# Performance work log

Hardware: AMD Instinct MI355X
Metric: run time of the kernel (lower is better)

Reference implementation:

```python
import jax, jax.numpy as jnp
import numpy as np

N = 50000      # nodes
E = 400000     # edges (avg degree 8)
N_IN = 256     # n_in_chan
N_HID = 256    # n_hid_chan


def gcn_conv(x, src, dst, W, b, n):
    """PyG GCNConv: D^{-1/2}(A+I)D^{-1/2} X W^T + b (add_self_loops=True, unit weights)."""
    h = x @ W.T                                           # [n, out]
    # degree over A + I: each node has a self loop (the initial ones) plus in-edges
    deg = jnp.ones((n,), h.dtype).at[dst].add(1.0)        # [n]
    dinv = jax.lax.rsqrt(deg)                             # deg >= 1 always
    norm = dinv[src] * dinv[dst]                          # [E]
    agg = jnp.zeros_like(h).at[dst].add(h[src] * norm[:, None])
    agg = agg + h * (dinv * dinv)[:, None]                # self-loop term, norm = dinv_i^2
    return agg + b


def setup_inputs() -> dict:
    key = jax.random.key(0)
    k1, k2, k3, k4 = jax.random.split(key, 4)
    x = jax.random.normal(k1, (N, N_IN + N_HID), dtype=jnp.float32)
    edge_index = jax.random.randint(k2, (2, E), 0, N, dtype=jnp.int64)
    s1 = 1.0 / np.sqrt(N_IN + N_HID)
    s2 = 1.0 / np.sqrt(N_HID)
    W1 = jax.random.normal(k3, (N_HID, N_IN + N_HID), dtype=jnp.float32) * s1
    W2 = jax.random.normal(k4, (N_HID, N_HID), dtype=jnp.float32) * s2
    b1 = jnp.zeros((N_HID,), jnp.float32)
    b2 = jnp.zeros((N_HID,), jnp.float32)
    return {"x": x, "edge_index": edge_index, "W1": W1, "b1": b1, "W2": W2, "b2": b2}


def reference(x, edge_index, W1, b1, W2, b2):
    src, dst = edge_index[0], edge_index[1]
    h = jax.nn.relu(gcn_conv(x, src, dst, W1, b1, N))
    return gcn_conv(h, src, dst, W2, b2, N)
```

## Files before the change

kernel.cpp:

```cpp
#include <hip/hip_runtime.h>
#include <hip/hip_bf16.h>

#define NN 50000
#define CH 256
#define SLOTS 96

typedef unsigned short u16;
typedef unsigned int   u32;

using short8 = __attribute__((ext_vector_type(8))) short;
using u16x8  = __attribute__((ext_vector_type(8))) unsigned short;
using f32x4  = __attribute__((ext_vector_type(4))) float;

static __device__ __forceinline__ float4 ld4(const float* p){ return *(const float4*)p; }

static __device__ __forceinline__ u16 f2b(float f){
  u32 u = __float_as_uint(f);
  u = (u + 0x7fffu + ((u >> 16) & 1u)) >> 16;
  return (u16)u;
}
static __device__ __forceinline__ float b2f(u16 b){
  return __uint_as_float(((u32)b) << 16);
}
static __device__ __forceinline__ int pkbf(float lo, float hi){
  __hip_bfloat162 h = __float22bfloat162_rn(make_float2(lo, hi));
  int r; __builtin_memcpy(&r, &h, 4); return r;
}


__global__ void ell_build_kernel(const int* __restrict__ src, const int* __restrict__ dst,
                                 int* __restrict__ deg, int* __restrict__ ell, int E,
                                 const float* __restrict__ W2, u16* __restrict__ W2bf, int w2n4){
  int T = gridDim.x * 256;
  int g = blockIdx.x*256 + threadIdx.x;
  if (g < E){
    int d = dst[g];
    int pos = atomicAdd(&deg[d], 1);
    if (pos < SLOTS) ell[(size_t)d*SLOTS + pos] = src[g];
  }
  for (int i = g; i < w2n4; i += T){
    float4 v = ld4(W2 + (size_t)i*4);
    ushort4 o; o.x=f2b(v.x); o.y=f2b(v.y); o.z=f2b(v.z); o.w=f2b(v.w);
    *(ushort4*)(W2bf + (size_t)i*4) = o;
  }
}


__global__ __launch_bounds__(256) void gemm_f32in_db_kernel(const float* __restrict__ A,
                                                            const float* __restrict__ B,
                                                            u16* __restrict__ C,
                                                            int M, int K){
  __shared__ u16 As[2][128*32];
  __shared__ u16 Bs[2][128*32];
  int tid = threadIdx.x;
  int wave = tid >> 6, lane = tid & 63;
  int bm = blockIdx.x, bn = blockIdx.y;

  int sr = tid >> 2;
  int sc = (tid & 3) * 8;
  int rA0 = bm*128 + sr;       if (rA0 > M-1) rA0 = M-1;
  int rA1 = bm*128 + 64 + sr;  if (rA1 > M-1) rA1 = M-1;
  const float* ga0 = A + (size_t)rA0*K + sc;
  const float* ga1 = A + (size_t)rA1*K + sc;
  const float* gb0 = B + (size_t)(bn*128 + sr)*K + sc;
  const float* gb1 = B + (size_t)(bn*128 + 64 + sr)*K + sc;

  int wm = wave & 1, wn = wave >> 1;
  int lm = lane & 15;
  int lk = (lane >> 4) * 8;

  f32x4 acc[4][4] = {};

  float4 a00,a01,a10,a11,b00,b01,b10,b11;
  auto LOADR = [&](int k0){
    a00 = ld4(ga0 + k0); a01 = ld4(ga0 + k0 + 4);
    a10 = ld4(ga1 + k0); a11 = ld4(ga1 + k0 + 4);
    b00 = ld4(gb0 + k0); b01 = ld4(gb0 + k0 + 4);
    b10 = ld4(gb1 + k0); b11 = ld4(gb1 + k0 + 4);
  };
  auto STORE = [&](int buf){
    int4 wa0 = { pkbf(a00.x,a00.y), pkbf(a00.z,a00.w), pkbf(a01.x,a01.y), pkbf(a01.z,a01.w) };
    int4 wa1 = { pkbf(a10.x,a10.y), pkbf(a10.z,a10.w), pkbf(a11.x,a11.y), pkbf(a11.z,a11.w) };
    int4 wb0 = { pkbf(b00.x,b00.y), pkbf(b00.z,b00.w), pkbf(b01.x,b01.y), pkbf(b01.z,b01.w) };
    int4 wb1 = { pkbf(b10.x,b10.y), pkbf(b10.z,b10.w), pkbf(b11.x,b11.y), pkbf(b11.z,b11.w) };
    *(int4*)&As[buf][(size_t)sr*32 + sc]      = wa0;
    *(int4*)&As[buf][(size_t)(64+sr)*32 + sc] = wa1;
    *(int4*)&Bs[buf][(size_t)sr*32 + sc]      = wb0;
    *(int4*)&Bs[buf][(size_t)(64+sr)*32 + sc] = wb1;
  };

  const int NIT = K >> 5;
  LOADR(0);
  STORE(0);
  if (NIT > 1) LOADR(32);
  __syncthreads();

  for (int it = 0; it < NIT; ++it){
    int buf = it & 1;
    short8 af[4], bfr[4];
    #pragma unroll
    for (int i=0;i<4;i++)
      af[i] = *(const short8*)&As[buf][(size_t)(wm*64 + i*16 + lm)*32 + lk];
    #pragma unroll
    for (int j=0;j<4;j++)
      bfr[j] = *(const short8*)&Bs[buf][(size_t)(wn*64 + j*16 + lm)*32 + lk];
    #pragma unroll
    for (int i=0;i<4;i++)
      #pragma unroll
      for (int j=0;j<4;j++)
        acc[i][j] = __builtin_amdgcn_mfma_f32_16x16x32_bf16(af[i], bfr[j], acc[i][j], 0, 0, 0);
    if (it + 1 < NIT){
      STORE(buf ^ 1);
      if (it + 2 < NIT) LOADR((it+2)*32);
    }
    __syncthreads();
  }

  int rb = (lane >> 4) * 4;
  #pragma unroll
  for (int i=0;i<4;i++){
    #pragma unroll
    for (int r=0;r<4;r++){
      int row = bm*128 + wm*64 + i*16 + rb + r;
      if (row < M){
        #pragma unroll
        for (int j=0;j<4;j++){
          int col = bn*128 + wn*64 + j*16 + lm;
          C[(size_t)row*CH + col] = f2b(acc[i][j][r]);
        }
      }
    }
  }
}


static __device__ __forceinline__ void gload_lds16(const u16* g, u16* l){
  __builtin_amdgcn_global_load_lds((const __attribute__((address_space(1))) void*)g,
                                   (__attribute__((address_space(3))) void*)l, 16, 0, 0);
}

__global__ __launch_bounds__(256) void gemm_mfma_kernel(const u16* __restrict__ A,
                                                        const u16* __restrict__ B,
                                                        u16* __restrict__ C,
                                                        int M, int K){
  __shared__ u16 As[128*32];
  __shared__ u16 Bs[128*32];
  int tid = threadIdx.x;
  int wave = tid >> 6, lane = tid & 63;
  int bm = blockIdx.x, bn = blockIdx.y;

  int sr = tid >> 2;
  int sc = (tid & 3) * 8;
  int ar0 = bm*128 + sr;       if (ar0 > M-1) ar0 = M-1;
  int ar1 = bm*128 + 64 + sr;  if (ar1 > M-1) ar1 = M-1;
  const u16* ga0 = A + (size_t)ar0*K + sc;
  const u16* ga1 = A + (size_t)ar1*K + sc;
  const u16* gb0 = B + (size_t)(bn*128 + sr)*K + sc;
  const u16* gb1 = B + (size_t)(bn*128 + 64 + sr)*K + sc;
  u16* la0 = As + (size_t)(wave*64)*8;
  u16* la1 = As + (size_t)(256 + wave*64)*8;
  u16* lb0 = Bs + (size_t)(wave*64)*8;
  u16* lb1 = Bs + (size_t)(256 + wave*64)*8;

  int wm = wave & 1, wn = wave >> 1;
  int lm = lane & 15;
  int lk = (lane >> 4) * 8;

  f32x4 acc[4][4] = {};

  for (int k0 = 0; k0 < K; k0 += 32){
    gload_lds16(ga0 + k0, la0);
    gload_lds16(ga1 + k0, la1);
    gload_lds16(gb0 + k0, lb0);
    gload_lds16(gb1 + k0, lb1);
    __syncthreads();
    short8 af[4], bfr[4];
    #pragma unroll
    for (int i=0;i<4;i++)
      af[i] = *(const short8*)&As[(size_t)(wm*64 + i*16 + lm)*32 + lk];
    #pragma unroll
    for (int j=0;j<4;j++)
      bfr[j] = *(const short8*)&Bs[(size_t)(wn*64 + j*16 + lm)*32 + lk];
    #pragma unroll
    for (int i=0;i<4;i++)
      #pragma unroll
      for (int j=0;j<4;j++)
        acc[i][j] = __builtin_amdgcn_mfma_f32_16x16x32_bf16(af[i], bfr[j], acc[i][j], 0, 0, 0);
    __syncthreads();
  }

  int rb = (lane >> 4) * 4;
  #pragma unroll
  for (int i=0;i<4;i++){
    #pragma unroll
    for (int r=0;r<4;r++){
      int row = bm*128 + wm*64 + i*16 + rb + r;
      if (row < M){
        #pragma unroll
        for (int j=0;j<4;j++){
          int col = bn*128 + wn*64 + j*16 + lm;
          C[(size_t)row*CH + col] = f2b(acc[i][j][r]);
        }
      }
    }
  }
}


template<bool RELU, bool OUTBF>
__global__ __launch_bounds__(256) void aggregate_kernel(const u16* __restrict__ h,
                                                        const float* __restrict__ bias,
                                                        const int* __restrict__ deg,
                                                        const int* __restrict__ ell,
                                                        void* __restrict__ outv, int n){
  int wave = threadIdx.x >> 6;
  int lane = threadIdx.x & 63;
  int i = blockIdx.x*4 + wave;
  if (i >= n) return;
  int half = lane >> 5;
  int c = (lane & 31) * 8;

  int degi = deg[i];
  float di = rsqrtf(1.0f + (float)degi);
  int m = degi < SLOTS ? degi : SLOTS;
  const int* row = ell + (size_t)i*SLOTS;

  float acc[8];
  #pragma unroll
  for (int k=0;k<8;k++) acc[k] = 0.f;

  int e = half;
  for (; e + 6 < m; e += 8){
    int s0 = row[e],   s1 = row[e+2], s2 = row[e+4], s3 = row[e+6];
    float n0 = rsqrtf(1.0f + (float)deg[s0]) * di;
    float n1 = rsqrtf(1.0f + (float)deg[s1]) * di;
    float n2 = rsqrtf(1.0f + (float)deg[s2]) * di;
    float n3 = rsqrtf(1.0f + (float)deg[s3]) * di;
    u16x8 h0 = *(const u16x8*)(h + (size_t)s0*CH + c);
    u16x8 h1 = *(const u16x8*)(h + (size_t)s1*CH + c);
    u16x8 h2 = *(const u16x8*)(h + (size_t)s2*CH + c);
    u16x8 h3 = *(const u16x8*)(h + (size_t)s3*CH + c);
    #pragma unroll
    for (int k=0;k<8;k++) acc[k] += b2f(h0[k])*n0;
    #pragma unroll
    for (int k=0;k<8;k++) acc[k] += b2f(h1[k])*n1;
    #pragma unroll
    for (int k=0;k<8;k++) acc[k] += b2f(h2[k])*n2;
    #pragma unroll
    for (int k=0;k<8;k++) acc[k] += b2f(h3[k])*n3;
  }
  for (; e < m; e += 2){
    int s0 = row[e];
    float n0 = rsqrtf(1.0f + (float)deg[s0]) * di;
    u16x8 h0 = *(const u16x8*)(h + (size_t)s0*CH + c);
    #pragma unroll
    for (int k=0;k<8;k++) acc[k] += b2f(h0[k])*n0;
  }

  if (half == 0){
    float w = di*di;
    float4 b0 = ld4(bias + c), b1 = ld4(bias + c + 4);
    u16x8 hv = *(const u16x8*)(h + (size_t)i*CH + c);
    acc[0] += b2f(hv[0])*w + b0.x; acc[1] += b2f(hv[1])*w + b0.y;
    acc[2] += b2f(hv[2])*w + b0.z; acc[3] += b2f(hv[3])*w + b0.w;
    acc[4] += b2f(hv[4])*w + b1.x; acc[5] += b2f(hv[5])*w + b1.y;
    acc[6] += b2f(hv[6])*w + b1.z; acc[7] += b2f(hv[7])*w + b1.w;
  }

  #pragma unroll
  for (int k=0;k<8;k++) acc[k] += __shfl_xor(acc[k], 32, 64);

  if (half == 0){
    if (RELU){
      #pragma unroll
      for (int k=0;k<8;k++) acc[k] = fmaxf(acc[k], 0.f);
    }
    if (OUTBF){
      u16x8 o;
      #pragma unroll
      for (int k=0;k<8;k++) o[k] = f2b(acc[k]);
      *(u16x8*)((u16*)outv + (size_t)i*CH + c) = o;
    } else {
      float* op = (float*)outv + (size_t)i*CH + c;
      *(float4*)op       = make_float4(acc[0],acc[1],acc[2],acc[3]);
      *(float4*)(op + 4) = make_float4(acc[4],acc[5],acc[6],acc[7]);
    }
  }
}


extern "C" void kernel_launch(void* const* d_in, const int* in_sizes, int n_in,
                              void* d_out, int out_size, void* d_ws, size_t ws_size,
                              hipStream_t stream){
  const float* x  = (const float*)d_in[0];
  const int*   ei = (const int*)d_in[1];
  const float* W1 = (const float*)d_in[2];
  const float* b1 = (const float*)d_in[3];
  const float* W2 = (const float*)d_in[4];
  const float* b2 = (const float*)d_in[5];
  float* out = (float*)d_out;

  const int n = NN;
  const int E = in_sizes[1] / 2;
  const int* src = ei;
  const int* dst = ei + E;
  const int KIN = in_sizes[0] / n;

  char* ws = (char*)d_ws;
  size_t off = 0;
  auto alloc = [&](size_t bytes)->char* {
    char* p = ws + off;
    off += (bytes + 255) & ~(size_t)255;
    return p;
  };
  u16*   h1bf   = (u16*)  alloc((size_t)n*CH*sizeof(u16));
  u16*   g2out  = (u16*)  alloc((size_t)n*CH*sizeof(u16));
  u16*   W2bf   = (u16*)  alloc((size_t)CH*CH*sizeof(u16));
  int*   deg    = (int*)  alloc((size_t)n*sizeof(int));
  int*   ell    = (int*)  alloc((size_t)n*SLOTS*sizeof(int));
  (void)ws_size;

  u16* g1out = (u16*)d_out;

  hipMemsetAsync(deg, 0, (size_t)n*sizeof(int), stream);
  ell_build_kernel<<<(E+255)/256, 256, 0, stream>>>(src, dst, deg, ell, E, W2, W2bf, CH*CH/4);

  dim3 gg((n+127)/128, CH/128);
  gemm_f32in_db_kernel<<<gg, 256, 0, stream>>>(x, W1, g1out, n, KIN);
  aggregate_kernel<true, true><<<(n+3)/4, 256, 0, stream>>>(g1out, b1, deg, ell, h1bf, n);

  gemm_mfma_kernel<<<gg, 256, 0, stream>>>(h1bf, W2bf, g2out, n, CH);
  aggregate_kernel<false, false><<<(n+3)/4, 256, 0, stream>>>(g2out, b2, deg, ell, out, n);
}
```

Before: 316.7 us.

## Shrink GEMM1 M-tile with deeper register prefetch; double-buffer GEMM2 LDS loads

GEMM1 drops its M tile from 128 to 64 rows per block and sets a launch-bounds occupancy hint of 4. It keeps two register stages of fp32 prefetch ahead of the bf16 LDS store, so global loads have more latency cover and more blocks fit per CU. GEMM2 now double-buffers its direct global-to-LDS loads, so the next K tile is fetched while MFMAs run on the current one. The cost is more LDS in GEMM2, lower reuse of B in GEMM1, and a GEMM1 loop unrolled by two that assumes an even tile count.

Result: slower. 328.8 us (+3.8%).

```diff
diff --git a/kernel.cpp b/kernel.cpp
--- a/kernel.cpp
+++ b/kernel.cpp
@@ -46,82 +46,91 @@
 }
 
 
-__global__ __launch_bounds__(256) void gemm_f32in_db_kernel(const float* __restrict__ A,
-                                                            const float* __restrict__ B,
-                                                            u16* __restrict__ C,
-                                                            int M, int K){
-  __shared__ u16 As[2][128*32];
+#define G1_LOAD(S, k0) do{                                              \
+    A##S##a = ld4(ga + (k0));      A##S##b = ld4(ga + (k0) + 4);        \
+    B##S##a = ld4(gb + (k0));      B##S##b = ld4(gb + (k0) + 4);        \
+    B##S##c = ld4(gb + (k0) + 8);  B##S##d = ld4(gb + (k0) + 12);       \
+  }while(0)
+
+#define G1_STORE(S, buf) do{                                            \
+    int4 wa = { pkbf(A##S##a.x,A##S##a.y), pkbf(A##S##a.z,A##S##a.w),   \
+                pkbf(A##S##b.x,A##S##b.y), pkbf(A##S##b.z,A##S##b.w) }; \
+    *(int4*)&As[buf][aoff] = wa;                                        \
+    int4 wb0 = { pkbf(B##S##a.x,B##S##a.y), pkbf(B##S##a.z,B##S##a.w),  \
+                 pkbf(B##S##b.x,B##S##b.y), pkbf(B##S##b.z,B##S##b.w) };\
+    int4 wb1 = { pkbf(B##S##c.x,B##S##c.y), pkbf(B##S##c.z,B##S##c.w),  \
+                 pkbf(B##S##d.x,B##S##d.y), pkbf(B##S##d.z,B##S##d.w) };\
+    *(int4*)&Bs[buf][boff]     = wb0;                                   \
+    *(int4*)&Bs[buf][boff + 8] = wb1;                                   \
+  }while(0)
+
+#define G1_COMPUTE(buf) do{                                             \
+    short8 af[2], bfr[4];                                               \
+    _Pragma("unroll")                                                   \
+    for (int i=0;i<2;i++)                                               \
+      af[i] = *(const short8*)&As[buf][(wm*32 + i*16 + lm)*32 + lk];    \
+    _Pragma("unroll")                                                   \
+    for (int j=0;j<4;j++)                                               \
+      bfr[j] = *(const short8*)&Bs[buf][(wn*64 + j*16 + lm)*32 + lk];   \
+    _Pragma("unroll")                                                   \
+    for (int i=0;i<2;i++)                                               \
+      _Pragma("unroll")                                                 \
+      for (int j=0;j<4;j++)                                             \
+        acc[i][j] = __builtin_amdgcn_mfma_f32_16x16x32_bf16(af[i], bfr[j], acc[i][j], 0, 0, 0); \
+  }while(0)
+
+__global__ __launch_bounds__(256, 4) void gemm1_kernel(const float* __restrict__ A,
+                                                       const float* __restrict__ B,
+                                                       u16* __restrict__ C,
+                                                       int M, int K){
+  __shared__ u16 As[2][64*32];
   __shared__ u16 Bs[2][128*32];
   int tid = threadIdx.x;
   int wave = tid >> 6, lane = tid & 63;
   int bm = blockIdx.x, bn = blockIdx.y;
 
-  int sr = tid >> 2;
-  int sc = (tid & 3) * 8;
-  int rA0 = bm*128 + sr;       if (rA0 > M-1) rA0 = M-1;
-  int rA1 = bm*128 + 64 + sr;  if (rA1 > M-1) rA1 = M-1;
-  const float* ga0 = A + (size_t)rA0*K + sc;
-  const float* ga1 = A + (size_t)rA1*K + sc;
-  const float* gb0 = B + (size_t)(bn*128 + sr)*K + sc;
-  const float* gb1 = B + (size_t)(bn*128 + 64 + sr)*K + sc;
+  int arow = bm*64 + (tid >> 2); if (arow > M-1) arow = M-1;
+  int akc  = (tid & 3) * 8;
+  const float* ga = A + (size_t)arow*K + akc;
+  int brow = bn*128 + (tid >> 1);
+  int bkc  = (tid & 1) * 16;
+  const float* gb = B + (size_t)brow*K + bkc;
+  int aoff = (tid>>2)*32 + akc;
+  int boff = (tid>>1)*32 + bkc;
 
   int wm = wave & 1, wn = wave >> 1;
   int lm = lane & 15;
   int lk = (lane >> 4) * 8;
 
-  f32x4 acc[4][4] = {};
-
-  float4 a00,a01,a10,a11,b00,b01,b10,b11;
-  auto LOADR = [&](int k0){
-    a00 = ld4(ga0 + k0); a01 = ld4(ga0 + k0 + 4);
-    a10 = ld4(ga1 + k0); a11 = ld4(ga1 + k0 + 4);
-    b00 = ld4(gb0 + k0); b01 = ld4(gb0 + k0 + 4);
-    b10 = ld4(gb1 + k0); b11 = ld4(gb1 + k0 + 4);
-  };
-  auto STORE = [&](int buf){
-    int4 wa0 = { pkbf(a00.x,a00.y), pkbf(a00.z,a00.w), pkbf(a01.x,a01.y), pkbf(a01.z,a01.w) };
-    int4 wa1 = { pkbf(a10.x,a10.y), pkbf(a10.z,a10.w), pkbf(a11.x,a11.y), pkbf(a11.z,a11.w) };
-    int4 wb0 = { pkbf(b00.x,b00.y), pkbf(b00.z,b00.w), pkbf(b01.x,b01.y), pkbf(b01.z,b01.w) };
-    int4 wb1 = { pkbf(b10.x,b10.y), pkbf(b10.z,b10.w), pkbf(b11.x,b11.y), pkbf(b11.z,b11.w) };
-    *(int4*)&As[buf][(size_t)sr*32 + sc]      = wa0;
-    *(int4*)&As[buf][(size_t)(64+sr)*32 + sc] = wa1;
-    *(int4*)&Bs[buf][(size_t)sr*32 + sc]      = wb0;
-    *(int4*)&Bs[buf][(size_t)(64+sr)*32 + sc] = wb1;
-  };
+  f32x4 acc[2][4] = {};
+
+  float4 A0a,A0b,B0a,B0b,B0c,B0d;
+  float4 A1a,A1b,B1a,B1b,B1c,B1d;
 
   const int NIT = K >> 5;
-  LOADR(0);
-  STORE(0);
-  if (NIT > 1) LOADR(32);
+  G1_LOAD(0, 0);
+  G1_LOAD(1, 32);
+  G1_STORE(0, 0);
+  G1_LOAD(0, 64);
   __syncthreads();
 
-  for (int it = 0; it < NIT; ++it){
-    int buf = it & 1;
-    short8 af[4], bfr[4];
-    #pragma unroll
-    for (int i=0;i<4;i++)
-      af[i] = *(const short8*)&As[buf][(size_t)(wm*64 + i*16 + lm)*32 + lk];
-    #pragma unroll
-    for (int j=0;j<4;j++)
-      bfr[j] = *(const short8*)&Bs[buf][(size_t)(wn*64 + j*16 + lm)*32 + lk];
-    #pragma unroll
-    for (int i=0;i<4;i++)
-      #pragma unroll
-      for (int j=0;j<4;j++)
-        acc[i][j] = __builtin_amdgcn_mfma_f32_16x16x32_bf16(af[i], bfr[j], acc[i][j], 0, 0, 0);
-    if (it + 1 < NIT){
-      STORE(buf ^ 1);
-      if (it + 2 < NIT) LOADR((it+2)*32);
-    }
+  for (int it = 0; it < NIT; it += 2){
+    G1_COMPUTE(0);
+    G1_STORE(1, 1);
+    if (it + 3 < NIT) G1_LOAD(1, (it+3)*32);
+    __syncthreads();
+    G1_COMPUTE(1);
+    if (it + 2 < NIT) G1_STORE(0, 0);
+    if (it + 4 < NIT) G1_LOAD(0, (it+4)*32);
     __syncthreads();
   }
 
   int rb = (lane >> 4) * 4;
   #pragma unroll
-  for (int i=0;i<4;i++){
+  for (int i=0;i<2;i++){
     #pragma unroll
     for (int r=0;r<4;r++){
-      int row = bm*128 + wm*64 + i*16 + rb + r;
+      int row = bm*64 + wm*32 + i*16 + rb + r;
       if (row < M){
         #pragma unroll
         for (int j=0;j<4;j++){
@@ -143,8 +152,8 @@
                                                         const u16* __restrict__ B,
                                                         u16* __restrict__ C,
                                                         int M, int K){
-  __shared__ u16 As[128*32];
-  __shared__ u16 Bs[128*32];
+  __shared__ u16 As[2][128*32];
+  __shared__ u16 Bs[2][128*32];
   int tid = threadIdx.x;
   int wave = tid >> 6, lane = tid & 63;
   int bm = blockIdx.x, bn = blockIdx.y;
@@ -157,10 +166,8 @@
   const u16* ga1 = A + (size_t)ar1*K + sc;
   const u16* gb0 = B + (size_t)(bn*128 + sr)*K + sc;
   const u16* gb1 = B + (size_t)(bn*128 + 64 + sr)*K + sc;
-  u16* la0 = As + (size_t)(wave*64)*8;
-  u16* la1 = As + (size_t)(256 + wave*64)*8;
-  u16* lb0 = Bs + (size_t)(wave*64)*8;
-  u16* lb1 = Bs + (size_t)(256 + wave*64)*8;
+  int la0 = wave*512;
+  int la1 = 2048 + wave*512;
 
   int wm = wave & 1, wn = wave >> 1;
   int lm = lane & 15;
@@ -168,19 +175,29 @@
 
   f32x4 acc[4][4] = {};
 
-  for (int k0 = 0; k0 < K; k0 += 32){
-    gload_lds16(ga0 + k0, la0);
-    gload_lds16(ga1 + k0, la1);
-    gload_lds16(gb0 + k0, lb0);
-    gload_lds16(gb1 + k0, lb1);
-    __syncthreads();
+  const int NT = K >> 5;
+  gload_lds16(ga0, &As[0][la0]);
+  gload_lds16(ga1, &As[0][la1]);
+  gload_lds16(gb0, &Bs[0][la0]);
+  gload_lds16(gb1, &Bs[0][la1]);
+  __syncthreads();
+
+  for (int t = 0; t < NT; ++t){
+    int buf = t & 1;
+    if (t + 1 < NT){
+      int k0 = (t+1)*32;
+      gload_lds16(ga0 + k0, &As[buf^1][la0]);
+      gload_lds16(ga1 + k0, &As[buf^1][la1]);
+      gload_lds16(gb0 + k0, &Bs[buf^1][la0]);
+      gload_lds16(gb1 + k0, &Bs[buf^1][la1]);
+    }
     short8 af[4], bfr[4];
     #pragma unroll
     for (int i=0;i<4;i++)
-      af[i] = *(const short8*)&As[(size_t)(wm*64 + i*16 + lm)*32 + lk];
+      af[i] = *(const short8*)&As[buf][(size_t)(wm*64 + i*16 + lm)*32 + lk];
     #pragma unroll
     for (int j=0;j<4;j++)
-      bfr[j] = *(const short8*)&Bs[(size_t)(wn*64 + j*16 + lm)*32 + lk];
+      bfr[j] = *(const short8*)&Bs[buf][(size_t)(wn*64 + j*16 + lm)*32 + lk];
     #pragma unroll
     for (int i=0;i<4;i++)
       #pragma unroll
@@ -325,10 +342,11 @@
   hipMemsetAsync(deg, 0, (size_t)n*sizeof(int), stream);
   ell_build_kernel<<<(E+255)/256, 256, 0, stream>>>(src, dst, deg, ell, E, W2, W2bf, CH*CH/4);
 
-  dim3 gg((n+127)/128, CH/128);
-  gemm_f32in_db_kernel<<<gg, 256, 0, stream>>>(x, W1, g1out, n, KIN);
+  dim3 g1((n+63)/64, CH/128);
+  gemm1_kernel<<<g1, 256, 0, stream>>>(x, W1, g1out, n, KIN);
   aggregate_kernel<true, true><<<(n+3)/4, 256, 0, stream>>>(g1out, b1, deg, ell, h1bf, n);
 
-  gemm_mfma_kernel<<<gg, 256, 0, stream>>>(h1bf, W2bf, g2out, n, CH);
+  dim3 g2((n+127)/128, CH/128);
+  gemm_mfma_kernel<<<g2, 256, 0, stream>>>(h1bf, W2bf, g2out, n, CH);
   aggregate_kernel<false, false><<<(n+3)/4, 256, 0, stream>>>(g2out, b2, deg, ell, out, n);
 }
```

## Deepen GEMM software pipelines with async LDS loads and prebuilt bf16 W1

Applied to the files above, without the earlier changes.

W1 is now converted to bf16 once in the prep kernel, so gemm1 streams it with global_load_lds directly into LDS instead of loading and converting fp32 in registers. Both GEMMs are fully unrolled with multi-stage LDS buffering: gemm1 uses a 4-stage B ring and a 2-stage A register/LDS pipeline, and gemm2 uses a 4-stage ring. Each stage uses a single vmcnt-gated barrier, so global loads overlap MFMA work instead of the load-sync-compute-sync pattern. The cost is K hardcoded to 512/256, more LDS per block (which may reduce occupancy), and fragile hand-counted waitcnt values.

Result: no change. 313.3 us (-1.1%).

```diff
diff --git a/kernel.cpp b/kernel.cpp
--- a/kernel.cpp
+++ b/kernel.cpp
@@ -4,6 +4,8 @@
 #define NN 50000
 #define CH 256
 #define SLOTS 96
+#define G1K 512
+#define G2K 256
 
 typedef unsigned short u16;
 typedef unsigned int   u32;
@@ -27,9 +29,20 @@
   int r; __builtin_memcpy(&r, &h, 4); return r;
 }
 
+static __device__ __forceinline__ void gload_lds16(const u16* g, u16* l){
+  __builtin_amdgcn_global_load_lds((const __attribute__((address_space(1))) void*)g,
+                                   (__attribute__((address_space(3))) void*)l, 16, 0, 0);
+}
+
+#define WBAR(vm) do{ \
+    asm volatile("s_waitcnt vmcnt(" #vm ") lgkmcnt(0)" ::: "memory"); \
+    __builtin_amdgcn_s_barrier(); \
+  }while(0)
+
 
 __global__ void ell_build_kernel(const int* __restrict__ src, const int* __restrict__ dst,
                                  int* __restrict__ deg, int* __restrict__ ell, int E,
+                                 const float* __restrict__ W1, u16* __restrict__ W1bf, int w1n4,
                                  const float* __restrict__ W2, u16* __restrict__ W2bf, int w2n4){
   int T = gridDim.x * 256;
   int g = blockIdx.x*256 + threadIdx.x;
@@ -38,6 +51,11 @@
     int pos = atomicAdd(&deg[d], 1);
     if (pos < SLOTS) ell[(size_t)d*SLOTS + pos] = src[g];
   }
+  for (int i = g; i < w1n4; i += T){
+    float4 v = ld4(W1 + (size_t)i*4);
+    ushort4 o; o.x=f2b(v.x); o.y=f2b(v.y); o.z=f2b(v.z); o.w=f2b(v.w);
+    *(ushort4*)(W1bf + (size_t)i*4) = o;
+  }
   for (int i = g; i < w2n4; i += T){
     float4 v = ld4(W2 + (size_t)i*4);
     ushort4 o; o.x=f2b(v.x); o.y=f2b(v.y); o.z=f2b(v.z); o.w=f2b(v.w);
@@ -46,24 +64,65 @@
 }
 
 
-__global__ __launch_bounds__(256) void gemm_f32in_db_kernel(const float* __restrict__ A,
-                                                            const float* __restrict__ B,
-                                                            u16* __restrict__ C,
-                                                            int M, int K){
+#define G1_GLB(kt, bb) do{ \
+    gload_lds16(gb0 + (kt)*32, &Bs[bb][wave*512]); \
+    gload_lds16(gb1 + (kt)*32, &Bs[bb][2048 + wave*512]); \
+  }while(0)
+
+#define G1_LA(S, k0) do{ \
+    A##S##a = ld4(ga0 + (k0)); A##S##b = ld4(ga0 + (k0) + 4); \
+    A##S##c = ld4(ga1 + (k0)); A##S##d = ld4(ga1 + (k0) + 4); \
+  }while(0)
+
+#define G1_SA(S) do{ \
+    int4 _w0 = { pkbf(A##S##a.x,A##S##a.y), pkbf(A##S##a.z,A##S##a.w), \
+                 pkbf(A##S##b.x,A##S##b.y), pkbf(A##S##b.z,A##S##b.w) }; \
+    int4 _w1 = { pkbf(A##S##c.x,A##S##c.y), pkbf(A##S##c.z,A##S##c.w), \
+                 pkbf(A##S##d.x,A##S##d.y), pkbf(A##S##d.z,A##S##d.w) }; \
+    *(int4*)&As[S][aoff0] = _w0; \
+    *(int4*)&As[S][aoff1] = _w1; \
+  }while(0)
+
+#define G1_COMP(ra, rb) do{ \
+    short8 af[4], bq[4]; \
+    _Pragma("unroll") \
+    for (int i=0;i<4;i++) af[i] = *(const short8*)&As[ra][(wm*64 + i*16 + lm)*32 + lk]; \
+    _Pragma("unroll") \
+    for (int j=0;j<4;j++) bq[j] = *(const short8*)&Bs[rb][(wn*64 + j*16 + lm)*32 + lk]; \
+    _Pragma("unroll") \
+    for (int i=0;i<4;i++) \
+      _Pragma("unroll") \
+      for (int j=0;j<4;j++) \
+        acc[i][j] = __builtin_amdgcn_mfma_f32_16x16x32_bf16(af[i], bq[j], acc[i][j], 0, 0, 0); \
+  }while(0)
+
+#define G1_BODY(t, ra, rb, ss, wb, vm) do{ \
+    if ((t)+2 < 16) G1_GLB((t)+2, wb); \
+    G1_COMP(ra, rb); \
+    if ((t)+1 < 16) G1_SA(ss); \
+    if ((t)+3 < 16) G1_LA(ss, ((t)+3)*32); \
+    WBAR(vm); \
+  }while(0)
+
+__global__ __launch_bounds__(256) void gemm1_kernel(const float* __restrict__ A,
+                                                    const u16* __restrict__ Bbf,
+                                                    u16* __restrict__ C, int M){
   __shared__ u16 As[2][128*32];
-  __shared__ u16 Bs[2][128*32];
+  __shared__ u16 Bs[4][128*32];
   int tid = threadIdx.x;
   int wave = tid >> 6, lane = tid & 63;
   int bm = blockIdx.x, bn = blockIdx.y;
 
   int sr = tid >> 2;
   int sc = (tid & 3) * 8;
-  int rA0 = bm*128 + sr;       if (rA0 > M-1) rA0 = M-1;
-  int rA1 = bm*128 + 64 + sr;  if (rA1 > M-1) rA1 = M-1;
-  const float* ga0 = A + (size_t)rA0*K + sc;
-  const float* ga1 = A + (size_t)rA1*K + sc;
-  const float* gb0 = B + (size_t)(bn*128 + sr)*K + sc;
-  const float* gb1 = B + (size_t)(bn*128 + 64 + sr)*K + sc;
+  int ar0 = bm*128 + sr;       if (ar0 > M-1) ar0 = M-1;
+  int ar1 = bm*128 + 64 + sr;  if (ar1 > M-1) ar1 = M-1;
+  const float* ga0 = A + (size_t)ar0*G1K + sc;
+  const float* ga1 = A + (size_t)ar1*G1K + sc;
+  const u16*   gb0 = Bbf + (size_t)(bn*128 + sr)*G1K + sc;
+  const u16*   gb1 = gb0 + (size_t)64*G1K;
+  int aoff0 = sr*32 + sc;
+  int aoff1 = (64+sr)*32 + sc;
 
   int wm = wave & 1, wn = wave >> 1;
   int lm = lane & 15;
@@ -71,50 +130,35 @@
 
   f32x4 acc[4][4] = {};
 
-  float4 a00,a01,a10,a11,b00,b01,b10,b11;
-  auto LOADR = [&](int k0){
-    a00 = ld4(ga0 + k0); a01 = ld4(ga0 + k0 + 4);
-    a10 = ld4(ga1 + k0); a11 = ld4(ga1 + k0 + 4);
-    b00 = ld4(gb0 + k0); b01 = ld4(gb0 + k0 + 4);
-    b10 = ld4(gb1 + k0); b11 = ld4(gb1 + k0 + 4);
-  };
-  auto STORE = [&](int buf){
-    int4 wa0 = { pkbf(a00.x,a00.y), pkbf(a00.z,a00.w), pkbf(a01.x,a01.y), pkbf(a01.z,a01.w) };
-    int4 wa1 = { pkbf(a10.x,a10.y), pkbf(a10.z,a10.w), pkbf(a11.x,a11.y), pkbf(a11.z,a11.w) };
-    int4 wb0 = { pkbf(b00.x,b00.y), pkbf(b00.z,b00.w), pkbf(b01.x,b01.y), pkbf(b01.z,b01.w) };
-    int4 wb1 = { pkbf(b10.x,b10.y), pkbf(b10.z,b10.w), pkbf(b11.x,b11.y), pkbf(b11.z,b11.w) };
-    *(int4*)&As[buf][(size_t)sr*32 + sc]      = wa0;
-    *(int4*)&As[buf][(size_t)(64+sr)*32 + sc] = wa1;
-    *(int4*)&Bs[buf][(size_t)sr*32 + sc]      = wb0;
-    *(int4*)&Bs[buf][(size_t)(64+sr)*32 + sc] = wb1;
-  };
-
-  const int NIT = K >> 5;
-  LOADR(0);
-  STORE(0);
-  if (NIT > 1) LOADR(32);
-  __syncthreads();
-
-  for (int it = 0; it < NIT; ++it){
-    int buf = it & 1;
-    short8 af[4], bfr[4];
-    #pragma unroll
-    for (int i=0;i<4;i++)
-      af[i] = *(const short8*)&As[buf][(size_t)(wm*64 + i*16 + lm)*32 + lk];
-    #pragma unroll
-    for (int j=0;j<4;j++)
-      bfr[j] = *(const short8*)&Bs[buf][(size_t)(wn*64 + j*16 + lm)*32 + lk];
-    #pragma unroll
-    for (int i=0;i<4;i++)
-      #pragma unroll
-      for (int j=0;j<4;j++)
-        acc[i][j] = __builtin_amdgcn_mfma_f32_16x16x32_bf16(af[i], bfr[j], acc[i][j], 0, 0, 0);
-    if (it + 1 < NIT){
-      STORE(buf ^ 1);
-      if (it + 2 < NIT) LOADR((it+2)*32);
-    }
-    __syncthreads();
-  }
+  float4 A0a,A0b,A0c,A0d;
+  float4 A1a,A1b,A1c,A1d;
+
+  G1_LA(0, 0);
+  G1_GLB(0, 0);
+  G1_LA(1, 32);
+  G1_GLB(1, 1);
+  asm volatile("s_waitcnt vmcnt(0)" ::: "memory");
+  G1_SA(0);
+  G1_LA(0, 64);
+  asm volatile("s_waitcnt lgkmcnt(0)" ::: "memory");
+  __builtin_amdgcn_s_barrier();
+
+  G1_BODY( 0, 0,0, 1, 2, 6);
+  G1_BODY( 1, 1,1, 0, 3, 6);
+  G1_BODY( 2, 0,2, 1, 0, 6);
+  G1_BODY( 3, 1,3, 0, 1, 6);
+  G1_BODY( 4, 0,0, 1, 2, 6);
+  G1_BODY( 5, 1,1, 0, 3, 6);
+  G1_BODY( 6, 0,2, 1, 0, 6);
+  G1_BODY( 7, 1,3, 0, 1, 6);
+  G1_BODY( 8, 0,0, 1, 2, 6);
+  G1_BODY( 9, 1,1, 0, 3, 6);
+  G1_BODY(10, 0,2, 1, 0, 6);
+  G1_BODY(11, 1,3, 0, 1, 6);
+  G1_BODY(12, 0,0, 1, 2, 6);
+  G1_BODY(13, 1,1, 0, 3, 2);
+  G1_BODY(14, 0,2, 1, 0, 0);
+  G1_COMP(1, 3);
 
   int rb = (lane >> 4) * 4;
   #pragma unroll
@@ -134,17 +178,31 @@
 }
 
 
-static __device__ __forceinline__ void gload_lds16(const u16* g, u16* l){
-  __builtin_amdgcn_global_load_lds((const __attribute__((address_space(1))) void*)g,
-                                   (__attribute__((address_space(3))) void*)l, 16, 0, 0);
-}
-
-__global__ __launch_bounds__(256) void gemm_mfma_kernel(const u16* __restrict__ A,
-                                                        const u16* __restrict__ B,
-                                                        u16* __restrict__ C,
-                                                        int M, int K){
-  __shared__ u16 As[128*32];
-  __shared__ u16 Bs[128*32];
+#define G2_GLB(kt, bb) do{ \
+    gload_lds16(ga0 + (kt)*32, &As2[bb][wave*512]); \
+    gload_lds16(ga1 + (kt)*32, &As2[bb][2048 + wave*512]); \
+    gload_lds16(gb0 + (kt)*32, &Bs2[bb][wave*512]); \
+    gload_lds16(gb1 + (kt)*32, &Bs2[bb][2048 + wave*512]); \
+  }while(0)
+
+#define G2_COMP(rb) do{ \
+    short8 af[4], bq[4]; \
+    _Pragma("unroll") \
+    for (int i=0;i<4;i++) af[i] = *(const short8*)&As2[rb][(wm*64 + i*16 + lm)*32 + lk]; \
+    _Pragma("unroll") \
+    for (int j=0;j<4;j++) bq[j] = *(const short8*)&Bs2[rb][(wn*64 + j*16 + lm)*32 + lk]; \
+    _Pragma("unroll") \
+    for (int i=0;i<4;i++) \
+      _Pragma("unroll") \
+      for (int j=0;j<4;j++) \
+        acc[i][j] = __builtin_amdgcn_mfma_f32_16x16x32_bf16(af[i], bq[j], acc[i][j], 0, 0, 0); \
+  }while(0)
+
+__global__ __launch_bounds__(256) void gemm2_kernel(const u16* __restrict__ A,
+                                                    const u16* __restrict__ B,
+                                                    u16* __restrict__ C, int M){
+  __shared__ u16 As2[4][128*32];
+  __shared__ u16 Bs2[4][128*32];
   int tid = threadIdx.x;
   int wave = tid >> 6, lane = tid & 63;
   int bm = blockIdx.x, bn = blockIdx.y;
@@ -153,14 +211,10 @@
   int sc = (tid & 3) * 8;
   int ar0 = bm*128 + sr;       if (ar0 > M-1) ar0 = M-1;
   int ar1 = bm*128 + 64 + sr;  if (ar1 > M-1) ar1 = M-1;
-  const u16* ga0 = A + (size_t)ar0*K + sc;
-  const u16* ga1 = A + (size_t)ar1*K + sc;
-  const u16* gb0 = B + (size_t)(bn*128 + sr)*K + sc;
-  const u16* gb1 = B + (size_t)(bn*128 + 64 + sr)*K + sc;
-  u16* la0 = As + (size_t)(wave*64)*8;
-  u16* la1 = As + (size_t)(256 + wave*64)*8;
-  u16* lb0 = Bs + (size_t)(wave*64)*8;
-  u16* lb1 = Bs + (size_t)(256 + wave*64)*8;
+  const u16* ga0 = A + (size_t)ar0*G2K + sc;
+  const u16* ga1 = A + (size_t)ar1*G2K + sc;
+  const u16* gb0 = B + (size_t)(bn*128 + sr)*G2K + sc;
+  const u16* gb1 = gb0 + (size_t)64*G2K;
 
   int wm = wave & 1, wn = wave >> 1;
   int lm = lane & 15;
@@ -168,26 +222,19 @@
 
   f32x4 acc[4][4] = {};
 
-  for (int k0 = 0; k0 < K; k0 += 32){
-    gload_lds16(ga0 + k0, la0);
-    gload_lds16(ga1 + k0, la1);
-    gload_lds16(gb0 + k0, lb0);
-    gload_lds16(gb1 + k0, lb1);
-    __syncthreads();
-    short8 af[4], bfr[4];
-    #pragma unroll
-    for (int i=0;i<4;i++)
-      af[i] = *(const short8*)&As[(size_t)(wm*64 + i*16 + lm)*32 + lk];
-    #pragma unroll
-    for (int j=0;j<4;j++)
-      bfr[j] = *(const short8*)&Bs[(size_t)(wn*64 + j*16 + lm)*32 + lk];
-    #pragma unroll
-    for (int i=0;i<4;i++)
-      #pragma unroll
-      for (int j=0;j<4;j++)
-        acc[i][j] = __builtin_amdgcn_mfma_f32_16x16x32_bf16(af[i], bfr[j], acc[i][j], 0, 0, 0);
-    __syncthreads();
-  }
+  G2_GLB(0, 0);
+  G2_GLB(1, 1);
+  asm volatile("s_waitcnt vmcnt(0)" ::: "memory");
+  __builtin_amdgcn_s_barrier();
+
+  G2_GLB(2, 2); G2_COMP(0); WBAR(4);
+  G2_GLB(3, 3); G2_COMP(1); WBAR(4);
+  G2_GLB(4, 0); G2_COMP(2); WBAR(4);
+  G2_GLB(5, 1); G2_COMP(3); WBAR(4);
+  G2_GLB(6, 2); G2_COMP(0); WBAR(4);
+  G2_GLB(7, 3); G2_COMP(1); WBAR(4);
+                G2_COMP(2); WBAR(0);
+                G2_COMP(3);
 
   int rb = (lane >> 4) * 4;
   #pragma unroll
@@ -304,7 +351,6 @@
   const int E = in_sizes[1] / 2;
   const int* src = ei;
   const int* dst = ei + E;
-  const int KIN = in_sizes[0] / n;
 
   char* ws = (char*)d_ws;
   size_t off = 0;
@@ -315,6 +361,7 @@
   };
   u16*   h1bf   = (u16*)  alloc((size_t)n*CH*sizeof(u16));
   u16*   g2out  = (u16*)  alloc((size_t)n*CH*sizeof(u16));
+  u16*   W1bf   = (u16*)  alloc((size_t)CH*G1K*sizeof(u16));
   u16*   W2bf   = (u16*)  alloc((size_t)CH*CH*sizeof(u16));
   int*   deg    = (int*)  alloc((size_t)n*sizeof(int));
   int*   ell    = (int*)  alloc((size_t)n*SLOTS*sizeof(int));
@@ -323,12 +370,14 @@
   u16* g1out = (u16*)d_out;
 
   hipMemsetAsync(deg, 0, (size_t)n*sizeof(int), stream);
-  ell_build_kernel<<<(E+255)/256, 256, 0, stream>>>(src, dst, deg, ell, E, W2, W2bf, CH*CH/4);
+  ell_build_kernel<<<(E+255)/256, 256, 0, stream>>>(src, dst, deg, ell, E,
+                                                    W1, W1bf, CH*G1K/4,
+                                                    W2, W2bf, CH*CH/4);
 
   dim3 gg((n+127)/128, CH/128);
-  gemm_f32in_db_kernel<<<gg, 256, 0, stream>>>(x, W1, g1out, n, KIN);
+  gemm1_kernel<<<gg, 256, 0, stream>>>(x, W1bf, g1out, n);
   aggregate_kernel<true, true><<<(n+3)/4, 256, 0, stream>>>(g1out, b1, deg, ell, h1bf, n);
 
-  gemm_mfma_kernel<<<gg, 256, 0, stream>>>(h1bf, W2bf, g2out, n, CH);
+  gemm2_kernel<<<gg, 256, 0, stream>>>(h1bf, W2bf, g2out, n);
   aggregate_kernel<false, false><<<(n+3)/4, 256, 0, stream>>>(g2out, b2, deg, ell, out, n);
 }
```
